# Kernel tuning notes

Measured on AMD Instinct MI355X. Metric: run time of the kernel, lower is better.

Reference implementation:

```python
import jax, jax.numpy as jnp
import numpy as np

N, M, D = 8192, 8192, 64


def setup_inputs() -> dict:
    key = jax.random.key(0)
    kx, ky, kg = jax.random.split(key, 3)
    x = jax.random.normal(kx, (N, D), dtype=jnp.float32)
    y = jax.random.normal(ky, (M, D), dtype=jnp.float32)
    # per-dimension gamma (anisotropic branch: gamma.numel() == d), positive
    gamma = jax.random.uniform(kg, (D,), dtype=jnp.float32, minval=0.1, maxval=2.0)
    return {"x": x, "y": y, "gamma": gamma}


def reference(x, y, gamma):
    # k(x, y) = exp(-sum_i gamma_i * (x_i - y_i)^2)
    # Fused form: gamma-weighted squared distance via the expansion
    # avoids materializing the (n, m, d) broadcast tensor.
    sq_x = jnp.sum(gamma * x * x, axis=-1)          # (n,)
    sq_y = jnp.sum(gamma * y * y, axis=-1)          # (m,)
    cross = jnp.einsum('nd,md->nm', x, gamma * y)   # (n, m)
    norm = sq_x[:, None] + sq_y[None, :] - 2.0 * cross
    return jnp.exp(-norm)
```

## Files before the change

kernel.cpp:

```cpp
#include <hip/hip_runtime.h>
#include <hip/hip_bf16.h>
#include <stdint.h>


#define KPAD 136
#define CSTRIDE 68

typedef __attribute__((ext_vector_type(8))) short bfrag8;
typedef __attribute__((ext_vector_type(4))) float facc4;

__device__ __forceinline__ unsigned short f2bf(float v) {
  uint32_t u = __float_as_uint(v);
  u += 0x7fffu + ((u >> 16) & 1u);
  return (unsigned short)(u >> 16);
}
__device__ __forceinline__ float bf2f(unsigned short h) {
  return __uint_as_float(((uint32_t)h) << 16);
}

__global__ __launch_bounds__(256, 4)
void qkm_rbf_kernel(const float* __restrict__ x, const float* __restrict__ y,
                    const float* __restrict__ gamma, float* __restrict__ out,
                    int M) {
  __shared__ __align__(16) unsigned short Ah[64 * KPAD];
  __shared__ __align__(16) unsigned short Bh[64 * KPAD];
  __shared__ float sqx[64];
  __shared__ float sqy[64];

  const int tid = threadIdx.x;
  const int n0 = blockIdx.y * 64;
  const int m0 = blockIdx.x * 64;

  {
    const float4* xv = (const float4*)(x + (size_t)n0 * 64);
    const float4* yv = (const float4*)(y + (size_t)m0 * 64);
    const float4* gv = (const float4*)gamma;
#pragma unroll
    for (int i = 0; i < 4; ++i) {
      const int f = tid + 256 * i;
      const int r = f >> 4;
      const int c = f & 15;
      const float4 g4 = gv[c];
      const float gj[4] = {g4.x, g4.y, g4.z, g4.w};

      {
        const float4 v = xv[f];
        const float vj[4] = {v.x, v.y, v.z, v.w};
        unsigned short h[4], lo[4];
        float s = 0.f;
#pragma unroll
        for (int j = 0; j < 4; ++j) {
          const float xval = vj[j];
          h[j] = f2bf(xval);
          lo[j] = f2bf(xval - bf2f(h[j]));
          s = fmaf(gj[j] * xval, xval, s);
        }
        uint2 hp, lp;
        hp.x = (uint32_t)h[0] | ((uint32_t)h[1] << 16);
        hp.y = (uint32_t)h[2] | ((uint32_t)h[3] << 16);
        lp.x = (uint32_t)lo[0] | ((uint32_t)lo[1] << 16);
        lp.y = (uint32_t)lo[2] | ((uint32_t)lo[3] << 16);
        *(uint2*)&Ah[r * KPAD + c * 4]      = hp;
        *(uint2*)&Ah[r * KPAD + 64 + c * 4] = lp;
        s += __shfl_xor(s, 1);
        s += __shfl_xor(s, 2);
        s += __shfl_xor(s, 4);
        s += __shfl_xor(s, 8);
        if (c == 0) sqx[r] = s;
      }
      {
        const float4 v = yv[f];
        const float vj[4] = {v.x, v.y, v.z, v.w};
        unsigned short h[4], lo[4];
        float s = 0.f;
#pragma unroll
        for (int j = 0; j < 4; ++j) {
          const float yval = vj[j];
          const float w = 2.f * gj[j] * yval;
          h[j] = f2bf(w);
          lo[j] = f2bf(w - bf2f(h[j]));
          s = fmaf(gj[j] * yval, yval, s);
        }
        uint2 hp, lp;
        hp.x = (uint32_t)h[0] | ((uint32_t)h[1] << 16);
        hp.y = (uint32_t)h[2] | ((uint32_t)h[3] << 16);
        lp.x = (uint32_t)lo[0] | ((uint32_t)lo[1] << 16);
        lp.y = (uint32_t)lo[2] | ((uint32_t)lo[3] << 16);
        *(uint2*)&Bh[r * KPAD + c * 4]      = hp;
        *(uint2*)&Bh[r * KPAD + 64 + c * 4] = lp;
        s += __shfl_xor(s, 1);
        s += __shfl_xor(s, 2);
        s += __shfl_xor(s, 4);
        s += __shfl_xor(s, 8);
        if (c == 0) sqy[r] = s;
      }
    }
  }
  __syncthreads();

  const int l  = tid & 63;
  const int wv = tid >> 6;
  const int rb = (wv & 1) * 32;
  const int cb = (wv >> 1) * 32;
  const int lr = l & 15;
  const int lq = l >> 4;

  facc4 acc[2][2] = {};

  const unsigned short* A0 = &Ah[(rb + lr) * KPAD + lq * 8];
  const unsigned short* A1 = A0 + 16 * KPAD;
  const unsigned short* B0 = &Bh[(cb + lr) * KPAD + lq * 8];
  const unsigned short* B1 = B0 + 16 * KPAD;

  const int akb[6] = {0, 32, 0, 32, 64, 96};
  const int bkb[6] = {0, 32, 64, 96, 0, 32};
#pragma unroll
  for (int p = 0; p < 6; ++p) {
    bfrag8 a0 = *(const bfrag8*)(A0 + akb[p]);
    bfrag8 a1 = *(const bfrag8*)(A1 + akb[p]);
    bfrag8 b0 = *(const bfrag8*)(B0 + bkb[p]);
    bfrag8 b1 = *(const bfrag8*)(B1 + bkb[p]);
    acc[0][0] = __builtin_amdgcn_mfma_f32_16x16x32_bf16(a0, b0, acc[0][0], 0, 0, 0);
    acc[0][1] = __builtin_amdgcn_mfma_f32_16x16x32_bf16(a0, b1, acc[0][1], 0, 0, 0);
    acc[1][0] = __builtin_amdgcn_mfma_f32_16x16x32_bf16(a1, b0, acc[1][0], 0, 0, 0);
    acc[1][1] = __builtin_amdgcn_mfma_f32_16x16x32_bf16(a1, b1, acc[1][1], 0, 0, 0);
  }

  __syncthreads();

  float* Ct = (float*)Ah;
  const float sy0 = sqy[cb + lr];
  const float sy1 = sqy[cb + 16 + lr];
#pragma unroll
  for (int ti = 0; ti < 2; ++ti) {
    const int rloc = rb + ti * 16 + lq * 4;
    const float4 sx = *(const float4*)&sqx[rloc];
    const float sxa[4] = {sx.x, sx.y, sx.z, sx.w};
#pragma unroll
    for (int q = 0; q < 4; ++q) {
      float* crow = Ct + (size_t)(rloc + q) * CSTRIDE;
      crow[cb + lr]      = __expf(acc[ti][0][q] - sxa[q] - sy0);
      crow[cb + 16 + lr] = __expf(acc[ti][1][q] - sxa[q] - sy1);
    }
  }
  __syncthreads();

#pragma unroll
  for (int i = 0; i < 4; ++i) {
    const int f = tid + 256 * i;
    const int row = f >> 4;
    const int c4 = f & 15;
    const float4 v = *(const float4*)(Ct + row * CSTRIDE + c4 * 4);
    *(float4*)(out + (size_t)(n0 + row) * M + m0 + c4 * 4) = v;
  }
}

extern "C" void kernel_launch(void* const* d_in, const int* in_sizes, int n_in,
                              void* d_out, int out_size, void* d_ws, size_t ws_size,
                              hipStream_t stream) {
  const float* x = (const float*)d_in[0];
  const float* y = (const float*)d_in[1];
  const float* g = (const float*)d_in[2];
  float* out = (float*)d_out;
  const int D = in_sizes[2];
  const int N = in_sizes[0] / D;
  const int M = in_sizes[1] / D;
  dim3 grid(M / 64, N / 64);
  qkm_rbf_kernel<<<grid, dim3(256), 0, stream>>>(x, y, g, out, M);
}
```

Before: 340.9 us.

## Precompute packed bf16 hi/lo operands in a prep kernel, skip LDS staging

Adds a prep kernel that converts x and gamma-scaled y into hi/lo bf16 splits once, stores them in the workspace in MFMA fragment order, and computes the weighted squared norms. The main kernel then loads its fragments straight from global memory into registers, dropping the per-tile conversion work, the LDS operand staging and one barrier. Output stores switch to nontemporal. The cost is an extra launch and a workspace round trip, and the main path only runs when the workspace is large enough; otherwise the old kernel is used as a fallback.

Result: faster. 278.5 us (-18.3%).

```diff
diff --git a/kernel.cpp b/kernel.cpp
--- a/kernel.cpp
+++ b/kernel.cpp
@@ -8,6 +8,7 @@
 
 typedef __attribute__((ext_vector_type(8))) short bfrag8;
 typedef __attribute__((ext_vector_type(4))) float facc4;
+typedef __attribute__((ext_vector_type(4))) float f32x4;
 
 __device__ __forceinline__ unsigned short f2bf(float v) {
   uint32_t u = __float_as_uint(v);
@@ -18,10 +19,128 @@
   return __uint_as_float(((uint32_t)h) << 16);
 }
 
+__global__ __launch_bounds__(256)
+void qkm_prep(const float* __restrict__ x, const float* __restrict__ y,
+              const float* __restrict__ gamma,
+              unsigned short* __restrict__ Apack, unsigned short* __restrict__ Bpack,
+              float* __restrict__ sqx, float* __restrict__ sqy, int N, int M) {
+  const int t = blockIdx.x * blockDim.x + threadIdx.x;
+  const bool isB = (t >= N);
+  const int r = isB ? (t - N) : t;
+  if (isB && r >= M) return;
+  const float4* src = (const float4*)((isB ? y : x) + (size_t)r * 64);
+  const float4* gv = (const float4*)gamma;
+  unsigned short* dst = isB ? Bpack : Apack;
+
+  unsigned short hi[64], lo[64];
+  float s = 0.f;
+#pragma unroll
+  for (int c = 0; c < 16; ++c) {
+    const float4 v = src[c];
+    const float4 g4 = gv[c];
+    const float vj[4] = {v.x, v.y, v.z, v.w};
+    const float gj[4] = {g4.x, g4.y, g4.z, g4.w};
+#pragma unroll
+    for (int j = 0; j < 4; ++j) {
+      const float val = vj[j];
+      s = fmaf(gj[j] * val, val, s);
+      const float wv = isB ? (2.f * gj[j] * val) : val;
+      const unsigned short h = f2bf(wv);
+      hi[c * 4 + j] = h;
+      lo[c * 4 + j] = f2bf(wv - bf2f(h));
+    }
+  }
+  (isB ? sqy : sqx)[r] = s;
+
+  const int p = r >> 4, lr = r & 15;
+#pragma unroll
+  for (int kb = 0; kb < 4; ++kb) {
+#pragma unroll
+    for (int lq = 0; lq < 4; ++lq) {
+      unsigned short tmp[8];
+#pragma unroll
+      for (int j = 0; j < 8; ++j) {
+        const int kk = kb * 32 + lq * 8 + j;
+        tmp[j] = (kk < 64) ? hi[kk] : lo[kk - 64];
+      }
+      uint4 pk;
+      pk.x = (uint32_t)tmp[0] | ((uint32_t)tmp[1] << 16);
+      pk.y = (uint32_t)tmp[2] | ((uint32_t)tmp[3] << 16);
+      pk.z = (uint32_t)tmp[4] | ((uint32_t)tmp[5] << 16);
+      pk.w = (uint32_t)tmp[6] | ((uint32_t)tmp[7] << 16);
+      *(uint4*)&dst[(((size_t)(p * 4 + kb)) * 64 + lq * 16 + lr) * 8] = pk;
+    }
+  }
+}
+
 __global__ __launch_bounds__(256, 4)
-void qkm_rbf_kernel(const float* __restrict__ x, const float* __restrict__ y,
-                    const float* __restrict__ gamma, float* __restrict__ out,
-                    int M) {
+void qkm_main(const unsigned short* __restrict__ Apack,
+              const unsigned short* __restrict__ Bpack,
+              const float* __restrict__ sqx, const float* __restrict__ sqy,
+              float* __restrict__ out, int M) {
+  __shared__ __align__(16) float Ct[64 * CSTRIDE];
+
+  const int tid = threadIdx.x;
+  const int l = tid & 63, wv = tid >> 6;
+  const int n0 = blockIdx.y * 64, m0 = blockIdx.x * 64;
+  const int rb = (wv & 1) * 32, cb = (wv >> 1) * 32;
+  const int lr = l & 15, lq = l >> 4;
+
+  const unsigned short* Af = Apack + (((size_t)((n0 + rb) >> 4) * 4) * 64 + l) * 8;
+  const unsigned short* Bf = Bpack + (((size_t)((m0 + cb) >> 4) * 4) * 64 + l) * 8;
+
+  bfrag8 a[2][4], b[2][4];
+#pragma unroll
+  for (int dp = 0; dp < 2; ++dp)
+#pragma unroll
+    for (int kb = 0; kb < 4; ++kb) {
+      a[dp][kb] = *(const bfrag8*)(Af + (size_t)(dp * 4 + kb) * 512);
+      b[dp][kb] = *(const bfrag8*)(Bf + (size_t)(dp * 4 + kb) * 512);
+    }
+
+  facc4 acc[2][2] = {};
+  const int ka[6] = {0, 1, 0, 1, 2, 3};
+  const int kc[6] = {0, 1, 2, 3, 0, 1};
+#pragma unroll
+  for (int s = 0; s < 6; ++s) {
+#pragma unroll
+    for (int dp = 0; dp < 2; ++dp)
+#pragma unroll
+      for (int dq = 0; dq < 2; ++dq)
+        acc[dp][dq] = __builtin_amdgcn_mfma_f32_16x16x32_bf16(
+            a[dp][ka[s]], b[dq][kc[s]], acc[dp][dq], 0, 0, 0);
+  }
+
+  const float sy0 = sqy[m0 + cb + lr];
+  const float sy1 = sqy[m0 + cb + 16 + lr];
+#pragma unroll
+  for (int ti = 0; ti < 2; ++ti) {
+    const int rloc = rb + ti * 16 + lq * 4;
+    const float4 sx = *(const float4*)&sqx[n0 + rloc];
+    const float sxa[4] = {sx.x, sx.y, sx.z, sx.w};
+#pragma unroll
+    for (int q = 0; q < 4; ++q) {
+      float* crow = Ct + (size_t)(rloc + q) * CSTRIDE;
+      crow[cb + lr]      = __expf(acc[ti][0][q] - sxa[q] - sy0);
+      crow[cb + 16 + lr] = __expf(acc[ti][1][q] - sxa[q] - sy1);
+    }
+  }
+  __syncthreads();
+
+#pragma unroll
+  for (int i = 0; i < 4; ++i) {
+    const int f = tid + 256 * i;
+    const int row = f >> 4;
+    const int c4 = f & 15;
+    const f32x4 v = *(const f32x4*)(Ct + row * CSTRIDE + c4 * 4);
+    __builtin_nontemporal_store(v, (f32x4*)(out + (size_t)(n0 + row) * M + m0 + c4 * 4));
+  }
+}
+
+__global__ __launch_bounds__(256, 4)
+void qkm_rbf_fallback(const float* __restrict__ x, const float* __restrict__ y,
+                      const float* __restrict__ gamma, float* __restrict__ out,
+                      int M) {
   __shared__ __align__(16) unsigned short Ah[64 * KPAD];
   __shared__ __align__(16) unsigned short Bh[64 * KPAD];
   __shared__ float sqx[64];
@@ -30,7 +149,6 @@
   const int tid = threadIdx.x;
   const int n0 = blockIdx.y * 64;
   const int m0 = blockIdx.x * 64;
-
   {
     const float4* xv = (const float4*)(x + (size_t)n0 * 64);
     const float4* yv = (const float4*)(y + (size_t)m0 * 64);
@@ -42,7 +160,6 @@
       const int c = f & 15;
       const float4 g4 = gv[c];
       const float gj[4] = {g4.x, g4.y, g4.z, g4.w};
-
       {
         const float4 v = xv[f];
         const float vj[4] = {v.x, v.y, v.z, v.w};
@@ -62,10 +179,8 @@
         lp.y = (uint32_t)lo[2] | ((uint32_t)lo[3] << 16);
         *(uint2*)&Ah[r * KPAD + c * 4]      = hp;
         *(uint2*)&Ah[r * KPAD + 64 + c * 4] = lp;
-        s += __shfl_xor(s, 1);
-        s += __shfl_xor(s, 2);
-        s += __shfl_xor(s, 4);
-        s += __shfl_xor(s, 8);
+        s += __shfl_xor(s, 1); s += __shfl_xor(s, 2);
+        s += __shfl_xor(s, 4); s += __shfl_xor(s, 8);
         if (c == 0) sqx[r] = s;
       }
       {
@@ -88,17 +203,15 @@
         lp.y = (uint32_t)lo[2] | ((uint32_t)lo[3] << 16);
         *(uint2*)&Bh[r * KPAD + c * 4]      = hp;
         *(uint2*)&Bh[r * KPAD + 64 + c * 4] = lp;
-        s += __shfl_xor(s, 1);
-        s += __shfl_xor(s, 2);
-        s += __shfl_xor(s, 4);
-        s += __shfl_xor(s, 8);
+        s += __shfl_xor(s, 1); s += __shfl_xor(s, 2);
+        s += __shfl_xor(s, 4); s += __shfl_xor(s, 8);
         if (c == 0) sqy[r] = s;
       }
     }
   }
   __syncthreads();
 
-  const int l  = tid & 63;
+  const int l = tid & 63;
   const int wv = tid >> 6;
   const int rb = (wv & 1) * 32;
   const int cb = (wv >> 1) * 32;
@@ -106,12 +219,10 @@
   const int lq = l >> 4;
 
   facc4 acc[2][2] = {};
-
   const unsigned short* A0 = &Ah[(rb + lr) * KPAD + lq * 8];
   const unsigned short* A1 = A0 + 16 * KPAD;
   const unsigned short* B0 = &Bh[(cb + lr) * KPAD + lq * 8];
   const unsigned short* B1 = B0 + 16 * KPAD;
-
   const int akb[6] = {0, 32, 0, 32, 64, 96};
   const int bkb[6] = {0, 32, 64, 96, 0, 32};
 #pragma unroll
@@ -125,7 +236,6 @@
     acc[1][0] = __builtin_amdgcn_mfma_f32_16x16x32_bf16(a1, b0, acc[1][0], 0, 0, 0);
     acc[1][1] = __builtin_amdgcn_mfma_f32_16x16x32_bf16(a1, b1, acc[1][1], 0, 0, 0);
   }
-
   __syncthreads();
 
   float* Ct = (float*)Ah;
@@ -144,7 +254,6 @@
     }
   }
   __syncthreads();
-
 #pragma unroll
   for (int i = 0; i < 4; ++i) {
     const int f = tid + 256 * i;
@@ -165,6 +274,24 @@
   const int D = in_sizes[2];
   const int N = in_sizes[0] / D;
   const int M = in_sizes[1] / D;
-  dim3 grid(M / 64, N / 64);
-  qkm_rbf_kernel<<<grid, dim3(256), 0, stream>>>(x, y, g, out, M);
-}
+
+  const size_t aBytes = (size_t)N * 128 * sizeof(unsigned short);
+  const size_t bBytes = (size_t)M * 128 * sizeof(unsigned short);
+  const size_t sxBytes = (size_t)N * sizeof(float);
+  const size_t syBytes = (size_t)M * sizeof(float);
+  const size_t need = aBytes + bBytes + sxBytes + syBytes + 256;
+
+  if (ws_size >= need) {
+    char* ws = (char*)d_ws;
+    unsigned short* Apack = (unsigned short*)ws;
+    unsigned short* Bpack = (unsigned short*)(ws + aBytes);
+    float* sqx = (float*)(ws + aBytes + bBytes);
+    float* sqy = (float*)(ws + aBytes + bBytes + sxBytes);
+    qkm_prep<<<(N + M + 255) / 256, 256, 0, stream>>>(x, y, g, Apack, Bpack, sqx, sqy, N, M);
+    dim3 grid(M / 64, N / 64);
+    qkm_main<<<grid, dim3(256), 0, stream>>>(Apack, Bpack, sqx, sqy, out, M);
+  } else {
+    dim3 grid(M / 64, N / 64);
+    qkm_rbf_fallback<<<grid, dim3(256), 0, stream>>>(x, y, g, out, M);
+  }
+}
```
